# Kernel tuning notes

Hardware: AMD Instinct MI355X
Metric: run time of the kernel (lower is better)

Reference implementation:

```python
import jax, jax.numpy as jnp
import numpy as np

D_IN = 4096
D_OUT = 4096
TOKENS = 8192


def setup_inputs() -> dict:
    key = jax.random.key(0)
    k_x, k_w = jax.random.split(key)
    x = jax.random.normal(k_x, (TOKENS, D_IN), dtype=jnp.float32)
    # int8 weight buffer (stored as int32 for jax friendliness; values in [-128,127))
    weight_i8 = jax.random.randint(k_w, (D_OUT, D_IN), -128, 127, dtype=jnp.int32)
    return {
        "x": x,
        "weight_i8": weight_i8,
        "weight_scale": jnp.array([0.01], dtype=jnp.float32),
        "weight_zero_point": jnp.zeros((1,), dtype=jnp.int32),
        "bias": jnp.zeros((D_OUT,), dtype=jnp.float32),
        "output_scale": jnp.array([0.5], dtype=jnp.float32),
        "output_zero_point": jnp.full((1,), 128, dtype=jnp.int32),
    }


def reference(x, weight_i8, weight_scale, weight_zero_point, bias,
              output_scale, output_zero_point):
    # NOTE: the torch module also computes torch.quantize_per_tensor(x, ...)
    # whose result is unused (dead code); it does not affect the output and
    # is omitted here.
    # Dequantize int8 weight: (w_int - zp) * scale  -> [D_OUT, D_IN] fp32
    w = (weight_i8.astype(jnp.float32)
         - weight_zero_point.astype(jnp.float32)) * weight_scale
    # Standard fp32 linear: [T, D_IN] @ [D_IN, D_OUT] + bias
    out = jnp.einsum("ti,oi->to", x, w) + bias
    # quantize_per_tensor(out, output_scale, output_zp, quint8).dequantize():
    # q = clamp(round(out/scale) + zp, 0, 255); deq = (q - zp) * scale
    zp = output_zero_point.astype(jnp.float32)
    q = jnp.clip(jnp.round(out / output_scale) + zp, 0.0, 255.0)
    return (q - zp) * output_scale
```

## Files before the change

kernel.cpp:

```cpp
#include <hip/hip_runtime.h>

#define TOKENS 8192
#define D_IN   4096
#define D_OUT  4096

typedef _Float16 f16;
typedef __attribute__((ext_vector_type(8))) _Float16 half8;
typedef __attribute__((ext_vector_type(4))) float    f32x4;
typedef __attribute__((address_space(3))) char       lds_char;


__global__ void cvt_x_kernel(const float* __restrict__ x, f16* __restrict__ xh) {
    size_t i = ((size_t)blockIdx.x * blockDim.x + threadIdx.x) * 4;
    float4 v = *reinterpret_cast<const float4*>(x + i);
    union { f16 h[4]; uint2 u; } p;
    p.h[0] = (f16)v.x; p.h[1] = (f16)v.y; p.h[2] = (f16)v.z; p.h[3] = (f16)v.w;
    *reinterpret_cast<uint2*>(xh + i) = p.u;
}

__global__ void cvt_w_kernel(const int* __restrict__ w, f16* __restrict__ wh,
                             const float* __restrict__ scale_p,
                             const int* __restrict__ zp_p) {
    size_t i = ((size_t)blockIdx.x * blockDim.x + threadIdx.x) * 4;
    float s = scale_p[0];
    float z = (float)zp_p[0];
    int4 v = *reinterpret_cast<const int4*>(w + i);
    union { f16 h[4]; uint2 u; } p;
    p.h[0] = (f16)(((float)v.x - z) * s);
    p.h[1] = (f16)(((float)v.y - z) * s);
    p.h[2] = (f16)(((float)v.z - z) * s);
    p.h[3] = (f16)(((float)v.w - z) * s);
    *reinterpret_cast<uint2*>(wh + i) = p.u;
}


#define BM 256
#define BN 256
#define BK 64
#define NT (D_IN / BK)
#define LDS_BUF   65536
#define LDS_B_OFF 32768

__device__ __forceinline__ void stage16(const f16* g, lds_char* l) {
    __builtin_amdgcn_global_load_lds(
        (const __attribute__((address_space(1))) void*)g,
        (__attribute__((address_space(3))) void*)l, 16, 0, 0);
}

#define LDS_LOAD8(p) (*(const __attribute__((address_space(3))) half8*)(p))

#define LOAD_AQ(DST, BUF, QM)                                               \
    do { _Pragma("unroll")                                                  \
        for (int fm = 0; fm < 4; ++fm) {                                    \
            int rr = wr * 128 + (QM) * 64 + fm * 16 + lr;                   \
            _Pragma("unroll")                                               \
            for (int ks = 0; ks < 2; ++ks)                                  \
                DST[fm][ks] = LDS_LOAD8((BUF) + rr * 128 +                  \
                                        ((cb0 + ks * 64) ^ swzr));          \
        } } while (0)

#define LOAD_BQ(DST, BUF, QN)                                               \
    do { _Pragma("unroll")                                                  \
        for (int fn = 0; fn < 2; ++fn) {                                    \
            int rr = wc * 64 + (QN) * 32 + fn * 16 + lr;                    \
            _Pragma("unroll")                                               \
            for (int ks = 0; ks < 2; ++ks)                                  \
                DST[fn][ks] = LDS_LOAD8((BUF) + rr * 128 +                  \
                                        ((cb0 + ks * 64) ^ swzr));          \
        } } while (0)

#define MFMA_Q(QM, QN, AV, BV)                                              \
    do { _Pragma("unroll")                                                  \
        for (int fm = 0; fm < 4; ++fm) {                                    \
            _Pragma("unroll")                                               \
            for (int fn = 0; fn < 2; ++fn) {                                \
                _Pragma("unroll")                                           \
                for (int ks = 0; ks < 2; ++ks)                              \
                    acc[(QM)*4+fm][(QN)*2+fn] =                             \
                        __builtin_amdgcn_mfma_f32_16x16x32_f16(             \
                            AV[fm][ks], BV[fn][ks],                         \
                            acc[(QM)*4+fm][(QN)*2+fn], 0, 0, 0);            \
            }                                                               \
        } } while (0)

#define FENCE()    asm volatile("" ::: "memory")
#define BAR()      __builtin_amdgcn_s_barrier()
#define VMCNT(N)   asm volatile("s_waitcnt vmcnt(" #N ")" ::: "memory")

__global__ __launch_bounds__(512, 2)
void gemm_pipe(const f16* __restrict__ A, const f16* __restrict__ B,
               const float* __restrict__ bias,
               const float* __restrict__ oscale_p, const int* __restrict__ ozp_p,
               float* __restrict__ C)
{
    __shared__ __align__(1024) char smem_[2 * LDS_BUF];
    lds_char* smem = (lds_char*)smem_;
    constexpr int K = D_IN, N = D_OUT;

    int nwg = gridDim.x;
    int cpx = nwg >> 3;
    int bid = blockIdx.x;
    int swz = (bid & 7) * cpx + (bid >> 3);
    int ntn = N / BN;
    int m0 = (swz / ntn) * BM;
    int n0 = (swz % ntn) * BN;

    int tid = threadIdx.x;
    int l   = tid & 63;
    int wv  = tid >> 6;
    int wr  = wv >> 2;
    int wc  = wv & 3;

    int srow = wv * 8 + (l >> 3);
    int scol = ((l & 7) ^ (l >> 3)) * 8;
    const f16* gA = A + (size_t)(m0 + srow) * K + scol;
    const f16* gB = B + (size_t)(n0 + srow) * K + scol;
    lds_char* dstbase = smem + wv * 1024 + l * 16;

    int lr   = l & 15;
    int swzr = (l & 7) << 4;
    int cb0  = (l >> 4) * 16;

    f32x4 acc[8][4] = {};
    half8 a0[4][2], a1[4][2], b0[2][2], b0n[2][2], b1[2][2];

    #pragma unroll
    for (int q = 0; q < 4; ++q) stage16(gA + (size_t)q * 64 * K, dstbase + q * 8192);
    #pragma unroll
    for (int q = 0; q < 4; ++q) stage16(gB + (size_t)q * 64 * K, dstbase + LDS_B_OFF + q * 8192);
    VMCNT(0);
    BAR();
    {
        const lds_char* bufA = smem;
        const lds_char* bufB = smem + LDS_B_OFF;
        LOAD_AQ(a0, bufA, 0);
        LOAD_BQ(b0, bufB, 0);
    }

    for (int t = 0; t < NT - 1; ++t) {
        const lds_char* bufA  = smem + (t & 1) * LDS_BUF;
        const lds_char* bufB  = bufA + LDS_B_OFF;
        const lds_char* bufAn = smem + ((t + 1) & 1) * LDS_BUF;
        const lds_char* bufBn = bufAn + LDS_B_OFF;
        lds_char* dst = dstbase + ((t + 1) & 1) * LDS_BUF;
        const f16* nA = gA + (size_t)(t + 1) * BK;
        const f16* nB = gB + (size_t)(t + 1) * BK;

        LOAD_BQ(b1, bufB, 1);
        stage16(nB,                      dst + LDS_B_OFF);
        stage16(nB + (size_t)64 * K,     dst + LDS_B_OFF + 8192);
        stage16(nB + (size_t)128 * K,    dst + LDS_B_OFF + 2 * 8192);
        stage16(nB + (size_t)192 * K,    dst + LDS_B_OFF + 3 * 8192);
        MFMA_Q(0, 0, a0, b0);
        MFMA_Q(0, 1, a0, b1);

        VMCNT(4);
        BAR();
        LOAD_AQ(a1, bufA, 1);
        stage16(nA,                      dst);
        stage16(nA + (size_t)128 * K,    dst + 2 * 8192);
        FENCE();
        stage16(nA + (size_t)64 * K,     dst + 8192);
        stage16(nA + (size_t)192 * K,    dst + 3 * 8192);
        MFMA_Q(1, 1, a1, b1);

        VMCNT(2);
        BAR();
        LOAD_AQ(a0, bufAn, 0);
        LOAD_BQ(b0n, bufBn, 0);
        MFMA_Q(1, 0, a1, b0);

        #pragma unroll
        for (int fn = 0; fn < 2; ++fn)
            #pragma unroll
            for (int ks = 0; ks < 2; ++ks)
                b0[fn][ks] = b0n[fn][ks];
    }

    {
        const lds_char* bufA = smem + ((NT - 1) & 1) * LDS_BUF;
        const lds_char* bufB = bufA + LDS_B_OFF;

        LOAD_BQ(b1, bufB, 1);
        MFMA_Q(0, 0, a0, b0);
        MFMA_Q(0, 1, a0, b1);

        VMCNT(0);
        BAR();
        LOAD_AQ(a1, bufA, 1);
        MFMA_Q(1, 1, a1, b1);
        MFMA_Q(1, 0, a1, b0);
    }

    float os  = oscale_p[0];
    float ozp = (float)ozp_p[0];
    float inv = 1.0f / os;
    #pragma unroll
    for (int qm = 0; qm < 2; ++qm) {
        #pragma unroll
        for (int fm = 0; fm < 4; ++fm) {
            int rowb = m0 + wr * 128 + qm * 64 + fm * 16 + (l >> 4) * 4;
            #pragma unroll
            for (int qn = 0; qn < 2; ++qn) {
                #pragma unroll
                for (int fn = 0; fn < 2; ++fn) {
                    int col = n0 + wc * 64 + qn * 32 + fn * 16 + lr;
                    float bv = bias[col];
                    f32x4 v = acc[qm * 4 + fm][qn * 2 + fn];
                    #pragma unroll
                    for (int j = 0; j < 4; ++j) {
                        float o = v[j] + bv;
                        float q = rintf(o * inv) + ozp;
                        q = fminf(fmaxf(q, 0.0f), 255.0f);
                        C[(size_t)(rowb + j) * N + col] = (q - ozp) * os;
                    }
                }
            }
        }
    }
}


extern "C" void kernel_launch(void* const* d_in, const int* in_sizes, int n_in,
                              void* d_out, int out_size, void* d_ws, size_t ws_size,
                              hipStream_t stream) {
    const float* x      = (const float*)d_in[0];
    const int*   w8     = (const int*)d_in[1];
    const float* wscale = (const float*)d_in[2];
    const int*   wzp    = (const int*)d_in[3];
    const float* bias   = (const float*)d_in[4];
    const float* oscale = (const float*)d_in[5];
    const int*   ozp    = (const int*)d_in[6];
    float* out = (float*)d_out;

    const size_t x_elems = (size_t)TOKENS * D_IN;
    const size_t w_elems = (size_t)D_OUT * D_IN;
    const size_t need = (x_elems + w_elems) * sizeof(f16);
    if (ws_size < need) return;

    f16* xh = (f16*)d_ws;
    f16* wh = xh + x_elems;

    {
        int blocks = (int)(x_elems / 4 / 256);
        cvt_x_kernel<<<blocks, 256, 0, stream>>>(x, xh);
    }
    {
        int blocks = (int)(w_elems / 4 / 256);
        cvt_w_kernel<<<blocks, 256, 0, stream>>>(w8, wh, wscale, wzp);
    }
    {
        int grid = (TOKENS / BM) * (D_OUT / BN);
        gemm_pipe<<<grid, 512, 0, stream>>>(xh, wh, bias, oscale, ozp, out);
    }
}
```

Measured before the change: 283.6 us.

## Restructure GEMM main loop with finer staged prefetch and MFMA priority boosts

```diff
diff --git a/kernel.cpp b/kernel.cpp
--- a/kernel.cpp
+++ b/kernel.cpp
@@ -83,15 +83,15 @@
             }                                                               \
         } } while (0)
 
-#define FENCE()    asm volatile("" ::: "memory")
 #define BAR()      __builtin_amdgcn_s_barrier()
 #define VMCNT(N)   asm volatile("s_waitcnt vmcnt(" #N ")" ::: "memory")
+#define PRIO(x)    __builtin_amdgcn_s_setprio(x)
 
 __global__ __launch_bounds__(512, 2)
-void gemm_pipe(const f16* __restrict__ A, const f16* __restrict__ B,
-               const float* __restrict__ bias,
-               const float* __restrict__ oscale_p, const int* __restrict__ ozp_p,
-               float* __restrict__ C)
+void gemm_ev(const f16* __restrict__ A, const f16* __restrict__ B,
+             const float* __restrict__ bias,
+             const float* __restrict__ oscale_p, const int* __restrict__ ozp_p,
+             float* __restrict__ C)
 {
     __shared__ __align__(1024) char smem_[2 * LDS_BUF];
     lds_char* smem = (lds_char*)smem_;
@@ -128,68 +128,66 @@
     for (int q = 0; q < 4; ++q) stage16(gA + (size_t)q * 64 * K, dstbase + q * 8192);
     #pragma unroll
     for (int q = 0; q < 4; ++q) stage16(gB + (size_t)q * 64 * K, dstbase + LDS_B_OFF + q * 8192);
-    VMCNT(0);
+    stage16(gA + (size_t)BK,                dstbase + LDS_BUF);
+    stage16(gA + (size_t)64 * K + BK,       dstbase + LDS_BUF + 8192);
+    VMCNT(2);
     BAR();
-    {
-        const lds_char* bufA = smem;
-        const lds_char* bufB = smem + LDS_B_OFF;
-        LOAD_AQ(a0, bufA, 0);
-        LOAD_BQ(b0, bufB, 0);
-    }
-
-    for (int t = 0; t < NT - 1; ++t) {
+    LOAD_AQ(a0, smem, 0);
+    LOAD_BQ(b0, (smem + LDS_B_OFF), 0);
+
+    for (int t = 0; t < NT; ++t) {
         const lds_char* bufA  = smem + (t & 1) * LDS_BUF;
         const lds_char* bufB  = bufA + LDS_B_OFF;
         const lds_char* bufAn = smem + ((t + 1) & 1) * LDS_BUF;
         const lds_char* bufBn = bufAn + LDS_B_OFF;
-        lds_char* dst = dstbase + ((t + 1) & 1) * LDS_BUF;
-        const f16* nA = gA + (size_t)(t + 1) * BK;
-        const f16* nB = gB + (size_t)(t + 1) * BK;
-
+        lds_char* dst1 = dstbase + ((t + 1) & 1) * LDS_BUF;
+        lds_char* dst2 = dstbase + (t & 1) * LDS_BUF;
+        const f16* nA  = gA + (size_t)(t + 1) * BK;
+        const f16* nB  = gB + (size_t)(t + 1) * BK;
+        const f16* n2A = gA + (size_t)(t + 2) * BK;
+
+        BAR();
         LOAD_BQ(b1, bufB, 1);
-        stage16(nB,                      dst + LDS_B_OFF);
-        stage16(nB + (size_t)64 * K,     dst + LDS_B_OFF + 8192);
-        stage16(nB + (size_t)128 * K,    dst + LDS_B_OFF + 2 * 8192);
-        stage16(nB + (size_t)192 * K,    dst + LDS_B_OFF + 3 * 8192);
-        MFMA_Q(0, 0, a0, b0);
-        MFMA_Q(0, 1, a0, b1);
+        if (t + 1 < NT) {
+            stage16(nA + (size_t)128 * K, dst1 + 2 * 8192);
+            stage16(nA + (size_t)192 * K, dst1 + 3 * 8192);
+            stage16(nB,                   dst1 + LDS_B_OFF);
+            stage16(nB + (size_t)64 * K,  dst1 + LDS_B_OFF + 8192);
+        }
+        PRIO(1); MFMA_Q(0, 0, a0, b0); PRIO(0);
+
+        BAR();
+        LOAD_AQ(a1, bufA, 1);
+        if (t + 1 < NT) {
+            stage16(nB + (size_t)128 * K, dst1 + LDS_B_OFF + 2 * 8192);
+            stage16(nB + (size_t)192 * K, dst1 + LDS_B_OFF + 3 * 8192);
+        }
+        PRIO(1); MFMA_Q(0, 1, a0, b1); PRIO(0);
 
         VMCNT(4);
         BAR();
-        LOAD_AQ(a1, bufA, 1);
-        stage16(nA,                      dst);
-        stage16(nA + (size_t)128 * K,    dst + 2 * 8192);
-        FENCE();
-        stage16(nA + (size_t)64 * K,     dst + 8192);
-        stage16(nA + (size_t)192 * K,    dst + 3 * 8192);
-        MFMA_Q(1, 1, a1, b1);
-
-        VMCNT(2);
-        BAR();
-        LOAD_AQ(a0, bufAn, 0);
-        LOAD_BQ(b0n, bufBn, 0);
-        MFMA_Q(1, 0, a1, b0);
-
-        #pragma unroll
-        for (int fn = 0; fn < 2; ++fn)
+        if (t + 1 < NT) LOAD_AQ(a0, bufAn, 0);
+        PRIO(1); MFMA_Q(1, 1, a1, b1); PRIO(0);
+        BAR();
+        if (t + 2 < NT) {
+            stage16(n2A,                  dst2);
+            stage16(n2A + (size_t)64 * K, dst2 + 8192);
+        }
+
+        if (t + 1 < NT) {
+            if (t + 2 < NT) { VMCNT(2); } else { VMCNT(0); }
+            BAR();
+            LOAD_BQ(b0n, bufBn, 0);
+            PRIO(1); MFMA_Q(1, 0, a1, b0); PRIO(0);
             #pragma unroll
-            for (int ks = 0; ks < 2; ++ks)
-                b0[fn][ks] = b0n[fn][ks];
-    }
-
-    {
-        const lds_char* bufA = smem + ((NT - 1) & 1) * LDS_BUF;
-        const lds_char* bufB = bufA + LDS_B_OFF;
-
-        LOAD_BQ(b1, bufB, 1);
-        MFMA_Q(0, 0, a0, b0);
-        MFMA_Q(0, 1, a0, b1);
-
-        VMCNT(0);
-        BAR();
-        LOAD_AQ(a1, bufA, 1);
-        MFMA_Q(1, 1, a1, b1);
-        MFMA_Q(1, 0, a1, b0);
+            for (int fn = 0; fn < 2; ++fn)
+                #pragma unroll
+                for (int ks = 0; ks < 2; ++ks)
+                    b0[fn][ks] = b0n[fn][ks];
+        } else {
+            BAR();
+            PRIO(1); MFMA_Q(1, 0, a1, b0); PRIO(0);
+        }
     }
 
     float os  = oscale_p[0];
@@ -251,6 +249,6 @@
     }
     {
         int grid = (TOKENS / BM) * (D_OUT / BN);
-        gemm_pipe<<<grid, 512, 0, stream>>>(xh, wh, bias, oscale, ozp, out);
-    }
-}
+        gemm_ev<<<grid, 512, 0, stream>>>(xh, wh, bias, oscale, ozp, out);
+    }
+}
```

Measured after the change: 291.3 us. 1.03x slower.

## Restructure GEMM main loop into four-phase pipeline with staggered LDS loads and setprio

Applied to the files above, without the earlier changes.

```diff
diff --git a/kernel.cpp b/kernel.cpp
--- a/kernel.cpp
+++ b/kernel.cpp
@@ -83,15 +83,22 @@
             }                                                               \
         } } while (0)
 
-#define FENCE()    asm volatile("" ::: "memory")
+#define COPYB(DST, SRC)                                                     \
+    do { _Pragma("unroll")                                                  \
+        for (int fn = 0; fn < 2; ++fn)                                      \
+            _Pragma("unroll")                                               \
+            for (int ks = 0; ks < 2; ++ks) DST[fn][ks] = SRC[fn][ks];       \
+    } while (0)
+
 #define BAR()      __builtin_amdgcn_s_barrier()
 #define VMCNT(N)   asm volatile("s_waitcnt vmcnt(" #N ")" ::: "memory")
+#define PRIO(x)    __builtin_amdgcn_s_setprio(x)
 
 __global__ __launch_bounds__(512, 2)
-void gemm_pipe(const f16* __restrict__ A, const f16* __restrict__ B,
-               const float* __restrict__ bias,
-               const float* __restrict__ oscale_p, const int* __restrict__ ozp_p,
-               float* __restrict__ C)
+void gemm_dl(const f16* __restrict__ A, const f16* __restrict__ B,
+             const float* __restrict__ bias,
+             const float* __restrict__ oscale_p, const int* __restrict__ ozp_p,
+             float* __restrict__ C)
 {
     __shared__ __align__(1024) char smem_[2 * LDS_BUF];
     lds_char* smem = (lds_char*)smem_;
@@ -122,74 +129,102 @@
     int cb0  = (l >> 4) * 16;
 
     f32x4 acc[8][4] = {};
-    half8 a0[4][2], a1[4][2], b0[2][2], b0n[2][2], b1[2][2];
+    half8 a0[4][2], a1[4][2];
+    half8 b0c[2][2], b0n[2][2], b1c[2][2], b1n[2][2];
 
     #pragma unroll
-    for (int q = 0; q < 4; ++q) stage16(gA + (size_t)q * 64 * K, dstbase + q * 8192);
+    for (int q = 0; q < 4; ++q)
+        stage16(gB + (size_t)q * 64 * K, dstbase + LDS_B_OFF + q * 8192);
     #pragma unroll
-    for (int q = 0; q < 4; ++q) stage16(gB + (size_t)q * 64 * K, dstbase + LDS_B_OFF + q * 8192);
+    for (int q = 0; q < 4; ++q)
+        stage16(gA + (size_t)q * 64 * K, dstbase + q * 8192);
     VMCNT(0);
     BAR();
+
     {
         const lds_char* bufA = smem;
         const lds_char* bufB = smem + LDS_B_OFF;
-        LOAD_AQ(a0, bufA, 0);
-        LOAD_BQ(b0, bufB, 0);
-    }
-
-    for (int t = 0; t < NT - 1; ++t) {
-        const lds_char* bufA  = smem + (t & 1) * LDS_BUF;
-        const lds_char* bufB  = bufA + LDS_B_OFF;
-        const lds_char* bufAn = smem + ((t + 1) & 1) * LDS_BUF;
-        const lds_char* bufBn = bufAn + LDS_B_OFF;
+        lds_char* dst = dstbase + LDS_BUF;
+        const f16* nA = gA + BK;
+        const f16* nB = gB + BK;
+
+        if (wc < 2) { LOAD_BQ(b0n, bufB, 0); LOAD_BQ(b1n, bufB, 1); }
+        stage16(nB,                   dst + LDS_B_OFF);
+        stage16(nB + (size_t)64 * K,  dst + LDS_B_OFF + 8192);
+        BAR();
+        if (wc >= 2) { LOAD_BQ(b0n, bufB, 0); LOAD_BQ(b1n, bufB, 1); }
+        COPYB(b1c, b1n);
+        stage16(nB + (size_t)128 * K, dst + LDS_B_OFF + 2 * 8192);
+        stage16(nB + (size_t)192 * K, dst + LDS_B_OFF + 3 * 8192);
+        BAR();
+        if (wr == 0) { LOAD_AQ(a0, bufA, 0); LOAD_AQ(a1, bufA, 1); }
+        COPYB(b0c, b0n);
+        stage16(nA,                   dst);
+        stage16(nA + (size_t)64 * K,  dst + 8192);
+        BAR();
+        if (wr == 1) { LOAD_AQ(a0, bufA, 0); LOAD_AQ(a1, bufA, 1); }
+        PRIO(1); MFMA_Q(0, 0, a0, b0c); PRIO(0);
+        stage16(nA + (size_t)128 * K, dst + 2 * 8192);
+        stage16(nA + (size_t)192 * K, dst + 3 * 8192);
+    }
+
+    for (int t = 1; t < NT - 1; ++t) {
+        const lds_char* bufA = smem + (t & 1) * LDS_BUF;
+        const lds_char* bufB = bufA + LDS_B_OFF;
         lds_char* dst = dstbase + ((t + 1) & 1) * LDS_BUF;
         const f16* nA = gA + (size_t)(t + 1) * BK;
         const f16* nB = gB + (size_t)(t + 1) * BK;
 
-        LOAD_BQ(b1, bufB, 1);
-        stage16(nB,                      dst + LDS_B_OFF);
-        stage16(nB + (size_t)64 * K,     dst + LDS_B_OFF + 8192);
-        stage16(nB + (size_t)128 * K,    dst + LDS_B_OFF + 2 * 8192);
-        stage16(nB + (size_t)192 * K,    dst + LDS_B_OFF + 3 * 8192);
-        MFMA_Q(0, 0, a0, b0);
-        MFMA_Q(0, 1, a0, b1);
-
-        VMCNT(4);
-        BAR();
-        LOAD_AQ(a1, bufA, 1);
-        stage16(nA,                      dst);
-        stage16(nA + (size_t)128 * K,    dst + 2 * 8192);
-        FENCE();
-        stage16(nA + (size_t)64 * K,     dst + 8192);
-        stage16(nA + (size_t)192 * K,    dst + 3 * 8192);
-        MFMA_Q(1, 1, a1, b1);
-
-        VMCNT(2);
-        BAR();
-        LOAD_AQ(a0, bufAn, 0);
-        LOAD_BQ(b0n, bufBn, 0);
-        MFMA_Q(1, 0, a1, b0);
-
-        #pragma unroll
-        for (int fn = 0; fn < 2; ++fn)
-            #pragma unroll
-            for (int ks = 0; ks < 2; ++ks)
-                b0[fn][ks] = b0n[fn][ks];
+        VMCNT(6); BAR();
+        if (wc < 2) { LOAD_BQ(b0n, bufB, 0); LOAD_BQ(b1n, bufB, 1); }
+        PRIO(1); MFMA_Q(0, 1, a0, b1c); PRIO(0);
+        stage16(nB,                   dst + LDS_B_OFF);
+        stage16(nB + (size_t)64 * K,  dst + LDS_B_OFF + 8192);
+
+        VMCNT(6); BAR();
+        if (wc >= 2) { LOAD_BQ(b0n, bufB, 0); LOAD_BQ(b1n, bufB, 1); }
+        PRIO(1); MFMA_Q(1, 1, a1, b1c); PRIO(0);
+        COPYB(b1c, b1n);
+        stage16(nB + (size_t)128 * K, dst + LDS_B_OFF + 2 * 8192);
+        stage16(nB + (size_t)192 * K, dst + LDS_B_OFF + 3 * 8192);
+
+        VMCNT(6); BAR();
+        PRIO(1); MFMA_Q(1, 0, a1, b0c); PRIO(0);
+        if (wr == 0) { LOAD_AQ(a0, bufA, 0); LOAD_AQ(a1, bufA, 1); }
+        COPYB(b0c, b0n);
+        stage16(nA,                   dst);
+        stage16(nA + (size_t)64 * K,  dst + 8192);
+
+        VMCNT(6); BAR();
+        if (wr == 1) { LOAD_AQ(a0, bufA, 0); LOAD_AQ(a1, bufA, 1); }
+        PRIO(1); MFMA_Q(0, 0, a0, b0c); PRIO(0);
+        stage16(nA + (size_t)128 * K, dst + 2 * 8192);
+        stage16(nA + (size_t)192 * K, dst + 3 * 8192);
     }
 
     {
         const lds_char* bufA = smem + ((NT - 1) & 1) * LDS_BUF;
         const lds_char* bufB = bufA + LDS_B_OFF;
 
-        LOAD_BQ(b1, bufB, 1);
-        MFMA_Q(0, 0, a0, b0);
-        MFMA_Q(0, 1, a0, b1);
-
-        VMCNT(0);
-        BAR();
-        LOAD_AQ(a1, bufA, 1);
-        MFMA_Q(1, 1, a1, b1);
-        MFMA_Q(1, 0, a1, b0);
+        VMCNT(6); BAR();
+        if (wc < 2) { LOAD_BQ(b0n, bufB, 0); LOAD_BQ(b1n, bufB, 1); }
+        PRIO(1); MFMA_Q(0, 1, a0, b1c); PRIO(0);
+        VMCNT(4); BAR();
+        if (wc >= 2) { LOAD_BQ(b0n, bufB, 0); LOAD_BQ(b1n, bufB, 1); }
+        PRIO(1); MFMA_Q(1, 1, a1, b1c); PRIO(0);
+        COPYB(b1c, b1n);
+        VMCNT(2); BAR();
+        PRIO(1); MFMA_Q(1, 0, a1, b0c); PRIO(0);
+        if (wr == 0) { LOAD_AQ(a0, bufA, 0); LOAD_AQ(a1, bufA, 1); }
+        COPYB(b0c, b0n);
+        VMCNT(0); BAR();
+        if (wr == 1) { LOAD_AQ(a0, bufA, 0); LOAD_AQ(a1, bufA, 1); }
+        PRIO(1);
+        MFMA_Q(0, 0, a0, b0c);
+        MFMA_Q(0, 1, a0, b1c);
+        MFMA_Q(1, 1, a1, b1c);
+        MFMA_Q(1, 0, a1, b0c);
+        PRIO(0);
     }
 
     float os  = oscale_p[0];
@@ -251,6 +286,6 @@
     }
     {
         int grid = (TOKENS / BM) * (D_OUT / BN);
-        gemm_pipe<<<grid, 512, 0, stream>>>(xh, wh, bias, oscale, ozp, out);
-    }
-}
+        gemm_dl<<<grid, 512, 0, stream>>>(xh, wh, bias, oscale, ozp, out);
+    }
+}
```

Result: slower. 525.0 us (+85.1%).
